# Optimization experiments

Measured on AMD Instinct MI355X. Metric: run time of the kernel, lower is better.

Reference implementation:

```python
import jax, jax.numpy as jnp
import numpy as np

B, T, N, DIM, HID, K = 512, 128, 18, 32, 64, 2
M = 2 * K + 1  # 2 supports (dual random walk) * K diffusion steps + identity


def setup_inputs() -> dict:
    key = jax.random.key(0)
    ks = jax.random.split(key, 8)
    s = 0.05
    x = jax.random.normal(ks[0], (B, T, N, DIM), dtype=jnp.float32)
    A = jax.random.uniform(ks[1], (2, N, N), dtype=jnp.float32)
    supports = A / jnp.sum(A, axis=-1, keepdims=True)  # row-normalized random-walk supports
    w_gate0 = jax.random.normal(ks[2], ((DIM + HID) * M, 2 * HID), dtype=jnp.float32) * s
    w_cand0 = jax.random.normal(ks[3], ((DIM + HID) * M, HID), dtype=jnp.float32) * s
    w_gate1 = jax.random.normal(ks[4], ((HID + HID) * M, 2 * HID), dtype=jnp.float32) * s
    w_cand1 = jax.random.normal(ks[5], ((HID + HID) * M, HID), dtype=jnp.float32) * s
    fc_w = jax.random.normal(ks[6], (HID, 1), dtype=jnp.float32) * s
    return {
        'x': x, 'supports': supports,
        'w_gate0': w_gate0, 'b_gate0': jnp.zeros((2 * HID,), jnp.float32),
        'w_cand0': w_cand0, 'b_cand0': jnp.zeros((HID,), jnp.float32),
        'w_gate1': w_gate1, 'b_gate1': jnp.zeros((2 * HID,), jnp.float32),
        'w_cand1': w_cand1, 'b_cand1': jnp.zeros((HID,), jnp.float32),
        'fc_w': fc_w, 'fc_b': jnp.zeros((1,), jnp.float32),
    }


def _dconv(x, supports, W, b):
    # x: [B, N, C] -> Chebyshev-style diffusion features, then dense projection
    feats = [x]
    for i in range(2):  # two supports (forward/backward random walk)
        S = supports[i]
        x0 = x
        x1 = jnp.einsum('nm,bmc->bnc', S, x0)
        feats.append(x1)
        for _ in range(2, K + 1):
            x2 = 2.0 * jnp.einsum('nm,bmc->bnc', S, x1) - x0
            feats.append(x2)
            x0, x1 = x1, x2
    h = jnp.concatenate(feats, axis=-1)  # [B, N, M*C]
    return h @ W + b


def _dcgru_cell(x, h, supports, wg, bg, wc, bc):
    ru = jax.nn.sigmoid(_dconv(jnp.concatenate([x, h], axis=-1), supports, wg, bg))
    r, u = jnp.split(ru, 2, axis=-1)
    c = jnp.tanh(_dconv(jnp.concatenate([x, r * h], axis=-1), supports, wc, bc))
    return u * h + (1.0 - u) * c


def reference(x, supports, w_gate0, b_gate0, w_cand0, b_cand0,
              w_gate1, b_gate1, w_cand1, b_cand1, fc_w, fc_b):
    xt = jnp.transpose(x, (1, 0, 2, 3))  # [T, B, N, DIM]
    h0 = jnp.zeros((x.shape[0], N, HID), x.dtype)

    def step(carry, xin):
        h_a, h_b = carry
        h_a = _dcgru_cell(xin, h_a, supports, w_gate0, b_gate0, w_cand0, b_cand0)
        h_b = _dcgru_cell(h_a, h_b, supports, w_gate1, b_gate1, w_cand1, b_cand1)
        return (h_a, h_b), h_b

    _, outs = jax.lax.scan(step, (h0, h0), xt)  # outs: [T, B, N, HID]
    last = outs[-1]  # [B, N, HID] (output[:, -1, :] in the torch code)
    logits = (jax.nn.relu(last) @ fc_w + fc_b)[..., 0]  # [B, N]; dropout is identity in eval
    return jnp.max(logits, axis=1)  # max-pool over nodes -> [B]
```

## Files before the change

### kernel.cpp

```cpp
#include <hip/hip_runtime.h>
#include <math.h>

#define NB 512
#define NT 128
#define NN 18
#define NDIM 32
#define NHID 64

typedef _Float16 half_t;
typedef _Float16 f16x4 __attribute__((ext_vector_type(4)));
typedef _Float16 f16x8 __attribute__((ext_vector_type(8)));
typedef float    f32x4 __attribute__((ext_vector_type(4)));

__device__ __forceinline__ float fast_sigmoid(float x) {
    return __builtin_amdgcn_rcpf(1.f + __expf(-x));
}
__device__ __forceinline__ float fast_tanh(float x) {
    float xc = fminf(fmaxf(x, -15.f), 15.f);
    float e  = __expf(2.f * xc);
    return 1.f - 2.f * __builtin_amdgcn_rcpf(e + 1.f);
}
__device__ __forceinline__ f32x4 mfma16(f16x8 a, f16x8 b, f32x4 c) {
    return __builtin_amdgcn_mfma_f32_16x16x32_f16(a, b, c, 0, 0, 0);
}

template <int KT, int CNT, int NCS>
__device__ __forceinline__ void mm1_u(const f16x8* __restrict__ Wf, int NTW,
                                      const half_t* Zf, half_t* Yf,
                                      int nt0, int lane) {
    constexpr int DEPTH = (CNT < 3) ? CNT : (KT == 3 ? CNT : 3);
    f16x8 A[2 * KT];
#pragma unroll
    for (int kt = 0; kt < KT; ++kt) {
        A[kt * 2 + 0] = *(const f16x8*)(Zf + (kt * 2 + 0) * 512 + lane * 8);
        A[kt * 2 + 1] = *(const f16x8*)(Zf + (kt * 2 + 1) * 512 + lane * 8);
    }
    f16x8 B[CNT][KT];
#pragma unroll
    for (int i = 0; i < DEPTH; ++i)
#pragma unroll
        for (int kt = 0; kt < KT; ++kt)
            B[i][kt] = Wf[(kt * NTW + nt0 + i) * 64 + lane];

    const int quad = lane >> 4, ln = lane & 15;
#pragma unroll
    for (int i = 0; i < CNT; ++i) {
        if (i + DEPTH < CNT) {
#pragma unroll
            for (int kt = 0; kt < KT; ++kt)
                B[i + DEPTH][kt] = Wf[(kt * NTW + nt0 + i + DEPTH) * 64 + lane];
        }
        const int ntp = nt0 + i;
        f32x4 ac0 = {0.f, 0.f, 0.f, 0.f};
        f32x4 ac1 = {0.f, 0.f, 0.f, 0.f};
#pragma unroll
        for (int kt = 0; kt < KT; ++kt) {
            ac0 = mfma16(A[kt * 2 + 0], B[i][kt], ac0);
            ac1 = mfma16(A[kt * 2 + 1], B[i][kt], ac1);
        }
        const int m  = ntp >> NCS;
        const int ot = ntp - (m << NCS);
        {
            const int k0 = 24 * m + quad * 4;
            f16x4 pk;
#pragma unroll
            for (int r = 0; r < 4; ++r) pk[r] = (half_t)ac0[r];
            *(f16x4*)(Yf + ((k0 >> 5) * 8 + ot) * 512 +
                      (((((k0 >> 3) & 3) << 4) | ln) * 8) + (k0 & 7)) = pk;
        }
        if (quad == 0) {
            const int k0 = 24 * m + 16;
            f16x4 pk;
#pragma unroll
            for (int r = 0; r < 4; ++r) pk[r] = (half_t)ac1[r];
            *(f16x4*)(Yf + ((k0 >> 5) * 8 + ot) * 512 +
                      (((((k0 >> 3) & 3) << 4) | ln) * 8) + (k0 & 7)) = pk;
        }
    }
}

__device__ __forceinline__ void mm2_gate(const half_t* Pc, const half_t* Yf,
                                         half_t* Zf, float bias,
                                         const float (*h)[NHID], float (*ub)[NHID],
                                         int DIMin, int wv, int lane) {
    const int nt2 = wv, quad = lane >> 4, ln = lane & 15;
    f32x4 a0 = {0.f, 0.f, 0.f, 0.f};
    f32x4 a1 = {0.f, 0.f, 0.f, 0.f};
#pragma unroll
    for (int kt = 0; kt < 4; ++kt) {
        f16x8 B  = *(const f16x8*)(Yf + (kt * 8 + nt2) * 512 + lane * 8);
        f16x8 A0 = *(const f16x8*)(Pc + (kt * 2 + 0) * 512 + lane * 8);
        f16x8 A1 = *(const f16x8*)(Pc + (kt * 2 + 1) * 512 + lane * 8);
        a0 = mfma16(A0, B, a0);
        a1 = mfma16(A1, B, a1);
    }
    const int o = nt2 * 16 + ln;
    if (o < NHID) {
        const int kZ = DIMin + o;
        const int base = ((kZ >> 5) * 2) * 512 + (((kZ >> 3) & 3) << 4) * 8 + (kZ & 7);
#pragma unroll
        for (int r = 0; r < 4; ++r) {
            int n = quad * 4 + r;
            float rv = fast_sigmoid(a0[r] + bias);
            Zf[base + (n & 15) * 8] = (half_t)(rv * h[n][o]);
        }
        if (quad == 0) {
#pragma unroll
            for (int r = 0; r < 2; ++r) {
                int n = 16 + r;
                float rv = fast_sigmoid(a1[r] + bias);
                Zf[base + 512 + (n & 15) * 8] = (half_t)(rv * h[n][o]);
            }
        }
    } else {
        const int oc = o - NHID;
#pragma unroll
        for (int r = 0; r < 4; ++r) ub[quad * 4 + r][oc] = fast_sigmoid(a0[r] + bias);
        if (quad == 0) {
#pragma unroll
            for (int r = 0; r < 2; ++r) ub[16 + r][oc] = fast_sigmoid(a1[r] + bias);
        }
    }
}

__device__ __forceinline__ void mm2_cand(const half_t* Pc, const half_t* Yf,
                                         float bias, float (*h)[NHID],
                                         const float (*ub)[NHID], int wv, int lane) {
    const int nt2 = wv & 3, mtA = wv >> 2;
    const int quad = lane >> 4;
    f32x4 a = {0.f, 0.f, 0.f, 0.f};
#pragma unroll
    for (int kt = 0; kt < 4; ++kt) {
        f16x8 B = *(const f16x8*)(Yf + (kt * 8 + nt2) * 512 + lane * 8);
        f16x8 A = *(const f16x8*)(Pc + (kt * 2 + mtA) * 512 + lane * 8);
        a = mfma16(A, B, a);
    }
    const int o = nt2 * 16 + (lane & 15);
#pragma unroll
    for (int r = 0; r < 4; ++r) {
        int n = mtA * 16 + quad * 4 + r;
        if (n < NN) {
            float cv = fast_tanh(a[r] + bias);
            float uv = ub[n][o];
            h[n][o] = uv * h[n][o] + (1.f - uv) * cv;
        }
    }
}

__global__ void pack_w(const float* __restrict__ W, f16x8* __restrict__ out,
                       int KT, int NTW, int ncol, int C) {
    int idx = blockIdx.x * blockDim.x + threadIdx.x;
    if (idx >= KT * NTW * 64) return;
    int lane = idx & 63, f = idx >> 6;
    int kt = f / NTW, ntp = f - kt * NTW;
    int ncol16 = ncol >> 4;
    int m = ntp / ncol16, ot = ntp - m * ncol16;
    int o = ot * 16 + (lane & 15);
    f16x8 v;
#pragma unroll
    for (int jj = 0; jj < 8; ++jj) {
        int c = kt * 32 + ((lane >> 4) << 3) + jj;
        v[jj] = (half_t)W[(m * C + c) * ncol + o];
    }
    out[idx] = v;
}

__global__ void pack_pcat(const float* __restrict__ sup, f16x8* __restrict__ out) {
    int tid = threadIdx.x;
    int lane = tid & 63, fidx = tid >> 6;
    int mtA = fidx & 1, kt2 = fidx >> 1;
    int n = mtA * 16 + (lane & 15);
    f16x8 v;
#pragma unroll 1
    for (int jj = 0; jj < 8; ++jj) {
        int k = kt2 * 32 + ((lane >> 4) << 3) + jj;
        int m = k / 24, j = k - m * 24;
        float val = 0.f;
        if (n < NN && j < NN && m < 5) {
            if (m == 0)      val = (n == j) ? 1.f : 0.f;
            else if (m == 1) val = sup[0 * 324 + n * 18 + j];
            else if (m == 3) val = sup[1 * 324 + n * 18 + j];
            else {
                const float* S = sup + ((m == 2) ? 0 : 1) * 324;
                float acc = 0.f;
                for (int l = 0; l < NN; ++l) acc += S[n * 18 + l] * S[l * 18 + j];
                val = 2.f * acc - ((n == j) ? 1.f : 0.f);
            }
        }
        v[jj] = (half_t)val;
    }
    out[fidx * 64 + lane] = v;
}

__global__ __launch_bounds__(512, 2) void dcrnn_kernel(
    const float* __restrict__ x,
    const f16x8* __restrict__ wg0, const float* __restrict__ bg0,
    const f16x8* __restrict__ wc0, const float* __restrict__ bc0,
    const f16x8* __restrict__ wg1, const float* __restrict__ bg1,
    const f16x8* __restrict__ wc1, const float* __restrict__ bc1,
    const f16x8* __restrict__ Pf,
    const float* __restrict__ fcw, const float* __restrict__ fcb,
    float* __restrict__ out) {
    __shared__ __align__(16) half_t Zf[8 * 512];
    __shared__ __align__(16) half_t Yf[32 * 512];
    __shared__ __align__(16) half_t Pc[8 * 512];
    __shared__ float h_a[NN][NHID];
    __shared__ float h_b[NN][NHID];
    __shared__ float ubuf[NN][NHID];

    const int tid  = threadIdx.x;
    const int lane = tid & 63;
    const int wv   = tid >> 6;
    const int b    = blockIdx.x;

    {
        f16x8 z = {0, 0, 0, 0, 0, 0, 0, 0};
        ((f16x8*)Zf)[tid] = z;
#pragma unroll
        for (int i = 0; i < 4; ++i) ((f16x8*)Yf)[tid + i * 512] = z;
        ((f16x8*)Pc)[tid] = Pf[tid];
        for (int i = tid; i < NN * NHID; i += 512) {
            ((float*)h_a)[i] = 0.f;
            ((float*)h_b)[i] = 0.f;
        }
    }

    const int gnt0 = wv * 5;
    const int cnt0 = (wv < 4) ? wv * 3 : 12 + (wv - 4) * 2;
    const int ln   = lane & 15;

    const float bgt0 = bg0[wv * 16 + ln];
    const float bct0 = bc0[(wv & 3) * 16 + ln];
    const float bgt1 = bg1[wv * 16 + ln];
    const float bct1 = bc1[(wv & 3) * 16 + ln];

    __syncthreads();

    const float* xb = x + (size_t)b * NT * NN * NDIM;

    for (int t = 0; t < NT; ++t) {
        const float* xt = xb + (size_t)t * NN * NDIM;

        for (int idx = tid; idx < NN * 12; idx += 512) {
            int n = idx / 12, c8 = idx - n * 12;
            int c = c8 * 8;
            const float* src = (c < NDIM) ? &xt[n * NDIM + c] : &h_a[n][c - NDIM];
            f16x8 o8;
#pragma unroll
            for (int q = 0; q < 8; ++q) o8[q] = (half_t)src[q];
            *(f16x8*)(Zf + ((c8 >> 2) * 2 + (n >> 4)) * 512 +
                      (((c8 & 3) << 4) | (n & 15)) * 8) = o8;
        }
        __syncthreads();
        mm1_u<3, 5, 3>(wg0, 40, Zf, Yf, gnt0, lane);
        __syncthreads();
        mm2_gate(Pc, Yf, Zf, bgt0, h_a, ubuf, 32, wv, lane);
        __syncthreads();
        if (wv < 4) mm1_u<3, 3, 2>(wc0, 20, Zf, Yf, cnt0, lane);
        else        mm1_u<3, 2, 2>(wc0, 20, Zf, Yf, cnt0, lane);
        __syncthreads();
        mm2_cand(Pc, Yf, bct0, h_a, ubuf, wv, lane);
        __syncthreads();

        for (int idx = tid; idx < NN * 16; idx += 512) {
            int n = idx >> 4, c8 = idx & 15;
            int c = c8 * 8;
            const float* src = (c < NHID) ? &h_a[n][c] : &h_b[n][c - NHID];
            f16x8 o8;
#pragma unroll
            for (int q = 0; q < 8; ++q) o8[q] = (half_t)src[q];
            *(f16x8*)(Zf + ((c8 >> 2) * 2 + (n >> 4)) * 512 +
                      (((c8 & 3) << 4) | (n & 15)) * 8) = o8;
        }
        __syncthreads();
        mm1_u<4, 5, 3>(wg1, 40, Zf, Yf, gnt0, lane);
        __syncthreads();
        mm2_gate(Pc, Yf, Zf, bgt1, h_b, ubuf, 64, wv, lane);
        __syncthreads();
        if (wv < 4) mm1_u<4, 3, 2>(wc1, 20, Zf, Yf, cnt0, lane);
        else        mm1_u<4, 2, 2>(wc1, 20, Zf, Yf, cnt0, lane);
        __syncthreads();
        mm2_cand(Pc, Yf, bct1, h_b, ubuf, wv, lane);
        __syncthreads();
    }

    if (tid < NN) {
        float acc = fcb[0];
#pragma unroll 1
        for (int c = 0; c < NHID; ++c)
            acc = fmaf(fmaxf(h_b[tid][c], 0.f), fcw[c], acc);
        ((float*)ubuf)[tid] = acc;
    }
    __syncthreads();
    if (tid == 0) {
        float m = -1e30f;
#pragma unroll
        for (int n = 0; n < NN; ++n) m = fmaxf(m, ((float*)ubuf)[n]);
        out[b] = m;
    }
}

extern "C" void kernel_launch(void* const* d_in, const int* in_sizes, int n_in,
                              void* d_out, int out_size, void* d_ws, size_t ws_size,
                              hipStream_t stream) {
    const float* x   = (const float*)d_in[0];
    const float* sup = (const float*)d_in[1];
    const float* wg0 = (const float*)d_in[2];
    const float* bg0 = (const float*)d_in[3];
    const float* wc0 = (const float*)d_in[4];
    const float* bc0 = (const float*)d_in[5];
    const float* wg1 = (const float*)d_in[6];
    const float* bg1 = (const float*)d_in[7];
    const float* wc1 = (const float*)d_in[8];
    const float* bc1 = (const float*)d_in[9];
    const float* fcw = (const float*)d_in[10];
    const float* fcb = (const float*)d_in[11];
    float* out = (float*)d_out;

    char* ws = (char*)d_ws;
    f16x8* wg0p = (f16x8*)(ws + 0);
    f16x8* wc0p = (f16x8*)(ws + 122880);
    f16x8* wg1p = (f16x8*)(ws + 184320);
    f16x8* wc1p = (f16x8*)(ws + 348160);
    f16x8* pfp  = (f16x8*)(ws + 430080);

    pack_w<<<dim3(30), dim3(256), 0, stream>>>(wg0, wg0p, 3, 40, 128, 96);
    pack_w<<<dim3(15), dim3(256), 0, stream>>>(wc0, wc0p, 3, 20, 64, 96);
    pack_w<<<dim3(40), dim3(256), 0, stream>>>(wg1, wg1p, 4, 40, 128, 128);
    pack_w<<<dim3(20), dim3(256), 0, stream>>>(wc1, wc1p, 4, 20, 64, 128);
    pack_pcat<<<dim3(1), dim3(512), 0, stream>>>(sup, pfp);

    dcrnn_kernel<<<dim3(NB), dim3(512), 0, stream>>>(
        x, wg0p, bg0, wc0p, bc0, wg1p, bg1, wc1p, bc1, pfp, fcw, fcb, out);
}
```

Baseline: 2.493 ms.

## Halve block to four waves and give each wave double the tile work

The recurrent kernel drops from 8 to 4 waves per block. Each wave now computes twice as many projection column tiles, and the gate stage computes both the r and u halves per wave. This removes the wave-dependent branches and the masked candidate rows, and it cuts barrier participants. The cost is less parallelism per block and more serial MFMA work and register pressure per wave, with a deeper weight prefetch set by the DEPTH change. With 512 blocks and two per CU, occupancy falls as well.

```diff
diff --git a/kernel.cpp b/kernel.cpp
--- a/kernel.cpp
+++ b/kernel.cpp
@@ -24,11 +24,12 @@
     return __builtin_amdgcn_mfma_f32_16x16x32_f16(a, b, c, 0, 0, 0);
 }
 
+
 template <int KT, int CNT, int NCS>
 __device__ __forceinline__ void mm1_u(const f16x8* __restrict__ Wf, int NTW,
                                       const half_t* Zf, half_t* Yf,
                                       int nt0, int lane) {
-    constexpr int DEPTH = (CNT < 3) ? CNT : (KT == 3 ? CNT : 3);
+    constexpr int DEPTH = (CNT <= 5) ? CNT : 4;
     f16x8 A[2 * KT];
 #pragma unroll
     for (int kt = 0; kt < KT; ++kt) {
@@ -79,68 +80,80 @@
     }
 }
 
-__device__ __forceinline__ void mm2_gate(const half_t* Pc, const half_t* Yf,
-                                         half_t* Zf, float bias,
-                                         const float (*h)[NHID], float (*ub)[NHID],
-                                         int DIMin, int wv, int lane) {
-    const int nt2 = wv, quad = lane >> 4, ln = lane & 15;
+__device__ __forceinline__ void mm2_gate4(const half_t* Pc, const half_t* Yf,
+                                          half_t* Zf, float bias_r, float bias_u,
+                                          const float (*h)[NHID], float (*ub)[NHID],
+                                          int DIMin, int wv, int lane) {
+    const int quad = lane >> 4, ln = lane & 15;
+    f32x4 a0r = {0.f, 0.f, 0.f, 0.f}, a1r = {0.f, 0.f, 0.f, 0.f};
+    f32x4 a0u = {0.f, 0.f, 0.f, 0.f}, a1u = {0.f, 0.f, 0.f, 0.f};
+#pragma unroll
+    for (int kt = 0; kt < 4; ++kt) {
+        f16x8 Br = *(const f16x8*)(Yf + (kt * 8 + wv) * 512 + lane * 8);
+        f16x8 Bu = *(const f16x8*)(Yf + (kt * 8 + wv + 4) * 512 + lane * 8);
+        f16x8 A0 = *(const f16x8*)(Pc + (kt * 2 + 0) * 512 + lane * 8);
+        f16x8 A1 = *(const f16x8*)(Pc + (kt * 2 + 1) * 512 + lane * 8);
+        a0r = mfma16(A0, Br, a0r);
+        a1r = mfma16(A1, Br, a1r);
+        a0u = mfma16(A0, Bu, a0u);
+        a1u = mfma16(A1, Bu, a1u);
+    }
+    const int o = wv * 16 + ln;
+    {
+        const int kZ = DIMin + o;
+        const int base = ((kZ >> 5) * 2) * 512 + (((kZ >> 3) & 3) << 4) * 8 + (kZ & 7);
+#pragma unroll
+        for (int r = 0; r < 4; ++r) {
+            int n = quad * 4 + r;
+            float rv = fast_sigmoid(a0r[r] + bias_r);
+            Zf[base + (n & 15) * 8] = (half_t)(rv * h[n][o]);
+        }
+        if (quad == 0) {
+#pragma unroll
+            for (int r = 0; r < 2; ++r) {
+                int n = 16 + r;
+                float rv = fast_sigmoid(a1r[r] + bias_r);
+                Zf[base + 512 + (n & 15) * 8] = (half_t)(rv * h[n][o]);
+            }
+        }
+    }
+    {
+#pragma unroll
+        for (int r = 0; r < 4; ++r) ub[quad * 4 + r][o] = fast_sigmoid(a0u[r] + bias_u);
+        if (quad == 0) {
+#pragma unroll
+            for (int r = 0; r < 2; ++r) ub[16 + r][o] = fast_sigmoid(a1u[r] + bias_u);
+        }
+    }
+}
+
+__device__ __forceinline__ void mm2_cand4(const half_t* Pc, const half_t* Yf,
+                                          float bias, float (*h)[NHID],
+                                          const float (*ub)[NHID], int wv, int lane) {
+    const int quad = lane >> 4, ln = lane & 15;
     f32x4 a0 = {0.f, 0.f, 0.f, 0.f};
     f32x4 a1 = {0.f, 0.f, 0.f, 0.f};
 #pragma unroll
     for (int kt = 0; kt < 4; ++kt) {
-        f16x8 B  = *(const f16x8*)(Yf + (kt * 8 + nt2) * 512 + lane * 8);
+        f16x8 B  = *(const f16x8*)(Yf + (kt * 8 + wv) * 512 + lane * 8);
         f16x8 A0 = *(const f16x8*)(Pc + (kt * 2 + 0) * 512 + lane * 8);
         f16x8 A1 = *(const f16x8*)(Pc + (kt * 2 + 1) * 512 + lane * 8);
         a0 = mfma16(A0, B, a0);
         a1 = mfma16(A1, B, a1);
     }
-    const int o = nt2 * 16 + ln;
-    if (o < NHID) {
-        const int kZ = DIMin + o;
-        const int base = ((kZ >> 5) * 2) * 512 + (((kZ >> 3) & 3) << 4) * 8 + (kZ & 7);
-#pragma unroll
-        for (int r = 0; r < 4; ++r) {
-            int n = quad * 4 + r;
-            float rv = fast_sigmoid(a0[r] + bias);
-            Zf[base + (n & 15) * 8] = (half_t)(rv * h[n][o]);
-        }
-        if (quad == 0) {
-#pragma unroll
-            for (int r = 0; r < 2; ++r) {
-                int n = 16 + r;
-                float rv = fast_sigmoid(a1[r] + bias);
-                Zf[base + 512 + (n & 15) * 8] = (half_t)(rv * h[n][o]);
-            }
-        }
-    } else {
-        const int oc = o - NHID;
-#pragma unroll
-        for (int r = 0; r < 4; ++r) ub[quad * 4 + r][oc] = fast_sigmoid(a0[r] + bias);
-        if (quad == 0) {
-#pragma unroll
-            for (int r = 0; r < 2; ++r) ub[16 + r][oc] = fast_sigmoid(a1[r] + bias);
-        }
-    }
-}
-
-__device__ __forceinline__ void mm2_cand(const half_t* Pc, const half_t* Yf,
-                                         float bias, float (*h)[NHID],
-                                         const float (*ub)[NHID], int wv, int lane) {
-    const int nt2 = wv & 3, mtA = wv >> 2;
-    const int quad = lane >> 4;
-    f32x4 a = {0.f, 0.f, 0.f, 0.f};
-#pragma unroll
-    for (int kt = 0; kt < 4; ++kt) {
-        f16x8 B = *(const f16x8*)(Yf + (kt * 8 + nt2) * 512 + lane * 8);
-        f16x8 A = *(const f16x8*)(Pc + (kt * 2 + mtA) * 512 + lane * 8);
-        a = mfma16(A, B, a);
-    }
-    const int o = nt2 * 16 + (lane & 15);
+    const int o = wv * 16 + ln;
 #pragma unroll
     for (int r = 0; r < 4; ++r) {
-        int n = mtA * 16 + quad * 4 + r;
-        if (n < NN) {
-            float cv = fast_tanh(a[r] + bias);
+        int n = quad * 4 + r;
+        float cv = fast_tanh(a0[r] + bias);
+        float uv = ub[n][o];
+        h[n][o] = uv * h[n][o] + (1.f - uv) * cv;
+    }
+    if (quad == 0) {
+#pragma unroll
+        for (int r = 0; r < 2; ++r) {
+            int n = 16 + r;
+            float cv = fast_tanh(a1[r] + bias);
             float uv = ub[n][o];
             h[n][o] = uv * h[n][o] + (1.f - uv) * cv;
         }
@@ -192,7 +205,7 @@
     out[fidx * 64 + lane] = v;
 }
 
-__global__ __launch_bounds__(512, 2) void dcrnn_kernel(
+__global__ __launch_bounds__(256, 2) void dcrnn_kernel(
     const float* __restrict__ x,
     const f16x8* __restrict__ wg0, const float* __restrict__ bg0,
     const f16x8* __restrict__ wc0, const float* __restrict__ bc0,
@@ -215,24 +228,28 @@
 
     {
         f16x8 z = {0, 0, 0, 0, 0, 0, 0, 0};
-        ((f16x8*)Zf)[tid] = z;
-#pragma unroll
-        for (int i = 0; i < 4; ++i) ((f16x8*)Yf)[tid + i * 512] = z;
-        ((f16x8*)Pc)[tid] = Pf[tid];
-        for (int i = tid; i < NN * NHID; i += 512) {
+        ((f16x8*)Zf)[tid]       = z;
+        ((f16x8*)Zf)[tid + 256] = z;
+#pragma unroll
+        for (int i = 0; i < 8; ++i) ((f16x8*)Yf)[tid + i * 256] = z;
+        ((f16x8*)Pc)[tid]       = Pf[tid];
+        ((f16x8*)Pc)[tid + 256] = Pf[tid + 256];
+        for (int i = tid; i < NN * NHID; i += 256) {
             ((float*)h_a)[i] = 0.f;
             ((float*)h_b)[i] = 0.f;
         }
     }
 
-    const int gnt0 = wv * 5;
-    const int cnt0 = (wv < 4) ? wv * 3 : 12 + (wv - 4) * 2;
+    const int gnt0 = wv * 10;
+    const int cnt0 = wv * 5;
     const int ln   = lane & 15;
 
-    const float bgt0 = bg0[wv * 16 + ln];
-    const float bct0 = bc0[(wv & 3) * 16 + ln];
-    const float bgt1 = bg1[wv * 16 + ln];
-    const float bct1 = bc1[(wv & 3) * 16 + ln];
+    const float bgr0 = bg0[wv * 16 + ln];
+    const float bgu0 = bg0[(wv + 4) * 16 + ln];
+    const float bct0 = bc0[wv * 16 + ln];
+    const float bgr1 = bg1[wv * 16 + ln];
+    const float bgu1 = bg1[(wv + 4) * 16 + ln];
+    const float bct1 = bc1[wv * 16 + ln];
 
     __syncthreads();
 
@@ -241,7 +258,7 @@
     for (int t = 0; t < NT; ++t) {
         const float* xt = xb + (size_t)t * NN * NDIM;
 
-        for (int idx = tid; idx < NN * 12; idx += 512) {
+        for (int idx = tid; idx < NN * 12; idx += 256) {
             int n = idx / 12, c8 = idx - n * 12;
             int c = c8 * 8;
             const float* src = (c < NDIM) ? &xt[n * NDIM + c] : &h_a[n][c - NDIM];
@@ -252,17 +269,16 @@
                       (((c8 & 3) << 4) | (n & 15)) * 8) = o8;
         }
         __syncthreads();
-        mm1_u<3, 5, 3>(wg0, 40, Zf, Yf, gnt0, lane);
-        __syncthreads();
-        mm2_gate(Pc, Yf, Zf, bgt0, h_a, ubuf, 32, wv, lane);
-        __syncthreads();
-        if (wv < 4) mm1_u<3, 3, 2>(wc0, 20, Zf, Yf, cnt0, lane);
-        else        mm1_u<3, 2, 2>(wc0, 20, Zf, Yf, cnt0, lane);
-        __syncthreads();
-        mm2_cand(Pc, Yf, bct0, h_a, ubuf, wv, lane);
-        __syncthreads();
-
-        for (int idx = tid; idx < NN * 16; idx += 512) {
+        mm1_u<3, 10, 3>(wg0, 40, Zf, Yf, gnt0, lane);
+        __syncthreads();
+        mm2_gate4(Pc, Yf, Zf, bgr0, bgu0, h_a, ubuf, 32, wv, lane);
+        __syncthreads();
+        mm1_u<3, 5, 2>(wc0, 20, Zf, Yf, cnt0, lane);
+        __syncthreads();
+        mm2_cand4(Pc, Yf, bct0, h_a, ubuf, wv, lane);
+        __syncthreads();
+
+        for (int idx = tid; idx < NN * 16; idx += 256) {
             int n = idx >> 4, c8 = idx & 15;
             int c = c8 * 8;
             const float* src = (c < NHID) ? &h_a[n][c] : &h_b[n][c - NHID];
@@ -273,14 +289,13 @@
                       (((c8 & 3) << 4) | (n & 15)) * 8) = o8;
         }
         __syncthreads();
-        mm1_u<4, 5, 3>(wg1, 40, Zf, Yf, gnt0, lane);
-        __syncthreads();
-        mm2_gate(Pc, Yf, Zf, bgt1, h_b, ubuf, 64, wv, lane);
-        __syncthreads();
-        if (wv < 4) mm1_u<4, 3, 2>(wc1, 20, Zf, Yf, cnt0, lane);
-        else        mm1_u<4, 2, 2>(wc1, 20, Zf, Yf, cnt0, lane);
-        __syncthreads();
-        mm2_cand(Pc, Yf, bct1, h_b, ubuf, wv, lane);
+        mm1_u<4, 10, 3>(wg1, 40, Zf, Yf, gnt0, lane);
+        __syncthreads();
+        mm2_gate4(Pc, Yf, Zf, bgr1, bgu1, h_b, ubuf, 64, wv, lane);
+        __syncthreads();
+        mm1_u<4, 5, 2>(wc1, 20, Zf, Yf, cnt0, lane);
+        __syncthreads();
+        mm2_cand4(Pc, Yf, bct1, h_b, ubuf, wv, lane);
         __syncthreads();
     }
 
@@ -330,6 +345,6 @@
     pack_w<<<dim3(20), dim3(256), 0, stream>>>(wc1, wc1p, 4, 20, 64, 128);
     pack_pcat<<<dim3(1), dim3(512), 0, stream>>>(sup, pfp);
 
-    dcrnn_kernel<<<dim3(NB), dim3(512), 0, stream>>>(
+    dcrnn_kernel<<<dim3(NB), dim3(256), 0, stream>>>(
         x, wg0p, bg0, wc0p, bc0, wg1p, bg1, wc1p, bc1, pfp, fcw, fcb, out);
 }
```

Result: slower. 5.447 ms (+118.5%).
